# Kernel tuning notes

Hardware: AMD Instinct MI355X
Metric: run time of the kernel (lower is better)

## Reference

```python
import jax, jax.numpy as jnp
import numpy as np

N_NODES = 50000
N_EDGES = 1600000
IN_C, HID_C, OUT_C = 64, 64, 7


def setup_inputs() -> dict:
    key = jax.random.key(0)
    ks = jax.random.split(key, 8)
    x = jax.random.normal(ks[0], (N_NODES, IN_C), dtype=jnp.float32)
    edge_index = jax.random.randint(ks[1], (2, N_EDGES), 0, N_NODES, dtype=jnp.int64)
    s_in = 1.0 / np.sqrt(IN_C)
    s_hid = 1.0 / np.sqrt(HID_C)
    W1 = jax.random.normal(ks[2], (HID_C, IN_C), dtype=jnp.float32) * s_in
    b1 = jnp.zeros((HID_C,), dtype=jnp.float32)
    W2 = jax.random.normal(ks[3], (HID_C, HID_C), dtype=jnp.float32) * s_hid
    b2 = jnp.zeros((HID_C,), dtype=jnp.float32)
    W3 = jax.random.normal(ks[4], (OUT_C, HID_C), dtype=jnp.float32) * s_hid
    b3 = jnp.zeros((OUT_C,), dtype=jnp.float32)
    return {"x": x, "edge_index": edge_index, "W1": W1, "b1": b1,
            "W2": W2, "b2": b2, "W3": W3, "b3": b3}


def _gcn_conv(x, src, dst, W, b):
    # GCNConv(normalize=False): lin -> sum-aggregate over incoming edges -> +bias
    h = x @ W.T                                   # [N, out]
    msg = h[src]                                  # gather source features [E, out]
    agg = jax.ops.segment_sum(msg, dst, num_segments=N_NODES)  # scatter-add
    return agg + b


def reference(x, edge_index, W1, b1, W2, b2, W3, b3):
    src, dst = edge_index[0], edge_index[1]
    h = jax.nn.relu(_gcn_conv(x, src, dst, W1, b1))   # dropout is identity in eval
    h = jax.nn.relu(_gcn_conv(h, src, dst, W2, b2))
    h = _gcn_conv(h, src, dst, W3, b3)
    return jax.nn.log_softmax(h, axis=-1)
```

## Files before the change

kernel.cpp:

```cpp
#include <hip/hip_runtime.h>
#include <math.h>

#define N_NODES 50000
#define N_EDGES 1600000
#define C 64
#define OUTC 7

#define NB 196
#define BCAP 10240
#define CHUNK 8192

#define ZROW N_NODES

typedef __attribute__((ext_vector_type(8))) short bf16x8;
typedef __attribute__((ext_vector_type(4))) float f32x4;
typedef __attribute__((ext_vector_type(2))) float f32x2;

__device__ __forceinline__ unsigned int pk_bf16(float a, float b) {
    unsigned int ua = __float_as_uint(a);
    ua = (ua + 0x7FFFu + ((ua >> 16) & 1u)) >> 16;
    unsigned int ub = __float_as_uint(b);
    ub = (ub + 0x7FFFu + ((ub >> 16) & 1u)) >> 16;
    return ua | (ub << 16);
}

union U4B8 { uint4 u; bf16x8 s; };

__global__ __launch_bounds__(256) void prep(const float* __restrict__ W1,
                                            const float* __restrict__ W2,
                                            unsigned int* __restrict__ Wb1,
                                            unsigned int* __restrict__ Wb2,
                                            int* __restrict__ gcursor) {
    const int b = blockIdx.x;
    const int tid = threadIdx.x;
    if (b < 8) {
        int idx = b * 256 + tid;
        float2 v = ((const float2*)W1)[idx];
        Wb1[idx] = pk_bf16(v.x, v.y);
    } else if (b < 16) {
        int idx = (b - 8) * 256 + tid;
        float2 v = ((const float2*)W2)[idx];
        Wb2[idx] = pk_bf16(v.x, v.y);
    } else {
        if (tid < NB) gcursor[tid] = 0;
    }
}

__global__ __launch_bounds__(256) void bin_kernel(const int* __restrict__ src,
                                                  const int* __restrict__ dst,
                                                  unsigned int* __restrict__ buckets,
                                                  int* __restrict__ gcursor) {
    __shared__ unsigned int staged[CHUNK];
    __shared__ int hist[NB], scanb[NB], cur[NB], baseb[NB];
    const int tid = threadIdx.x;
    const int base = blockIdx.x * CHUNK;
    int n = N_EDGES - base; if (n > CHUNK) n = CHUNK;

    for (int b = tid; b < NB; b += 256) { hist[b] = 0; cur[b] = 0; }
    __syncthreads();

    const int4* src4 = (const int4*)(src + base);
    const int4* dst4 = (const int4*)(dst + base);
    unsigned int v[32];
    int nv = n >> 2;
#pragma unroll
    for (int k = 0; k < 8; ++k) {
        int i4 = k * 256 + tid;
        if (i4 < nv) {
            int4 s4 = src4[i4];
            int4 d4 = dst4[i4];
            unsigned int d0 = (unsigned int)d4.x, d1 = (unsigned int)d4.y;
            unsigned int d2 = (unsigned int)d4.z, d3 = (unsigned int)d4.w;
            v[k * 4 + 0] = (d0 << 16) | (unsigned int)s4.x;
            v[k * 4 + 1] = (d1 << 16) | (unsigned int)s4.y;
            v[k * 4 + 2] = (d2 << 16) | (unsigned int)s4.z;
            v[k * 4 + 3] = (d3 << 16) | (unsigned int)s4.w;
            atomicAdd(&hist[d0 >> 8], 1);
            atomicAdd(&hist[d1 >> 8], 1);
            atomicAdd(&hist[d2 >> 8], 1);
            atomicAdd(&hist[d3 >> 8], 1);
        }
    }
    __syncthreads();
    if (tid == 0) {
        int run = 0;
        for (int b = 0; b < NB; ++b) { scanb[b] = run; run += hist[b]; }
    }
    __syncthreads();
#pragma unroll
    for (int k = 0; k < 8; ++k) {
        int i4 = k * 256 + tid;
        if (i4 < nv) {
#pragma unroll
            for (int q = 0; q < 4; ++q) {
                unsigned int w = v[k * 4 + q];
                int b = w >> 24;
                int p = scanb[b] + atomicAdd(&cur[b], 1);
                staged[p] = w;
            }
        }
    }
    __syncthreads();
    if (tid < NB) baseb[tid] = atomicAdd(&gcursor[tid], hist[tid]);
    __syncthreads();
    for (int i = tid; i < n; i += 256) {
        unsigned int w = staged[i];
        int b = w >> 24;
        buckets[(size_t)b * BCAP + baseb[b] + (i - scanb[b])] = w;
    }
}

__global__ __launch_bounds__(256) void build_csr(const unsigned int* __restrict__ buckets,
                                                 const int* __restrict__ gcursor,
                                                 unsigned int* __restrict__ csr,
                                                 int* __restrict__ off) {
    __shared__ int hist[256], part[256], offx[256], cur[256];
    __shared__ int gl[NB];
    __shared__ int s_cnt, s_base;
    const int tid = threadIdx.x;
    const int b = blockIdx.x;

    hist[tid] = 0;
    cur[tid] = 0;
    if (tid < NB) gl[tid] = gcursor[tid];
    __syncthreads();
    if (tid == 0) {
        int bs = 0;
        for (int i = 0; i < b; ++i) bs += gl[i];
        s_base = bs;
        s_cnt = gl[b];
    }
    __syncthreads();
    const int cnt = s_cnt;
    const int gbase = s_base;
    const unsigned int* bk = buckets + (size_t)b * BCAP;

    for (int i = tid; i < cnt; i += 256) {
        atomicAdd(&hist[(bk[i] >> 16) & 255], 1);
    }
    __syncthreads();
    part[tid] = hist[tid];
    __syncthreads();
    for (int d = 1; d < 256; d <<= 1) {
        int t = (tid >= d) ? part[tid - d] : 0;
        __syncthreads();
        part[tid] += t;
        __syncthreads();
    }
    offx[tid] = (tid == 0) ? 0 : part[tid - 1];
    __syncthreads();
    int node = b * 256 + tid;
    if (node < N_NODES) off[node] = gbase + offx[tid];
    if (b == NB - 1 && tid == 0) off[N_NODES] = gbase + cnt;
    for (int i = tid; i < cnt; i += 256) {
        unsigned int w = bk[i];
        int dl = (w >> 16) & 255;
        int p = offx[dl] + atomicAdd(&cur[dl], 1);
        csr[gbase + p] = w & 0xFFFFu;
    }
}


__global__ __launch_bounds__(256) void linear64_mfma_x(const float* __restrict__ x,
                                                       const unsigned int* __restrict__ Wb,
                                                       unsigned int* __restrict__ out) {
    if (blockIdx.x == 0 && threadIdx.x < 32)
        out[(size_t)ZROW * 32 + threadIdx.x] = 0u;
    const int wave = threadIdx.x >> 6;
    const int lane = threadIdx.x & 63;
    const int quad = lane >> 4;
    const int l16  = lane & 15;
    const int rbase = blockIdx.x * 64 + wave * 16;
    if (rbase >= N_NODES) return;

    U4B8 bfrag[4][2];
#pragma unroll
    for (int ct = 0; ct < 4; ++ct)
#pragma unroll
        for (int kt = 0; kt < 2; ++kt)
            bfrag[ct][kt].u = *(const uint4*)(Wb + (ct * 16 + l16) * 32 + kt * 16 + quad * 4);

    U4B8 afrag[2];
#pragma unroll
    for (int kt = 0; kt < 2; ++kt) {
        const float4* xp = (const float4*)(x + (size_t)(rbase + l16) * 64 + kt * 32 + quad * 8);
        float4 f0 = xp[0];
        float4 f1 = xp[1];
        afrag[kt].u.x = pk_bf16(f0.x, f0.y);
        afrag[kt].u.y = pk_bf16(f0.z, f0.w);
        afrag[kt].u.z = pk_bf16(f1.x, f1.y);
        afrag[kt].u.w = pk_bf16(f1.z, f1.w);
    }

    f32x4 acc[4];
#pragma unroll
    for (int ct = 0; ct < 4; ++ct) {
        f32x4 z = {0.f, 0.f, 0.f, 0.f};
        z = __builtin_amdgcn_mfma_f32_16x16x32_bf16(afrag[0].s, bfrag[ct][0].s, z, 0, 0, 0);
        z = __builtin_amdgcn_mfma_f32_16x16x32_bf16(afrag[1].s, bfrag[ct][1].s, z, 0, 0, 0);
        acc[ct] = z;
    }

    const int colp = l16 >> 1;
    const bool even = (l16 & 1) == 0;
#pragma unroll
    for (int ct = 0; ct < 4; ++ct) {
#pragma unroll
        for (int i = 0; i < 4; ++i) {
            float v = acc[ct][i];
            float p = __shfl_xor(v, 1, 64);
            if (even) {
                int row = rbase + quad * 4 + i;
                out[(size_t)row * 32 + ct * 8 + colp] = pk_bf16(v, p);
            }
        }
    }
}

__global__ __launch_bounds__(256) void linear64_mfma(const unsigned int* __restrict__ in,
                                                     const unsigned int* __restrict__ Wb,
                                                     unsigned int* __restrict__ out) {
    if (blockIdx.x == 0 && threadIdx.x < 32)
        out[(size_t)ZROW * 32 + threadIdx.x] = 0u;
    const int wave = threadIdx.x >> 6;
    const int lane = threadIdx.x & 63;
    const int quad = lane >> 4;
    const int l16  = lane & 15;
    const int rbase = blockIdx.x * 64 + wave * 16;
    if (rbase >= N_NODES) return;

    U4B8 bfrag[4][2];
#pragma unroll
    for (int ct = 0; ct < 4; ++ct)
#pragma unroll
        for (int kt = 0; kt < 2; ++kt)
            bfrag[ct][kt].u = *(const uint4*)(Wb + (ct * 16 + l16) * 32 + kt * 16 + quad * 4);

    U4B8 afrag[2];
#pragma unroll
    for (int kt = 0; kt < 2; ++kt)
        afrag[kt].u = *(const uint4*)(in + (size_t)(rbase + l16) * 32 + kt * 16 + quad * 4);

    f32x4 acc[4];
#pragma unroll
    for (int ct = 0; ct < 4; ++ct) {
        f32x4 z = {0.f, 0.f, 0.f, 0.f};
        z = __builtin_amdgcn_mfma_f32_16x16x32_bf16(afrag[0].s, bfrag[ct][0].s, z, 0, 0, 0);
        z = __builtin_amdgcn_mfma_f32_16x16x32_bf16(afrag[1].s, bfrag[ct][1].s, z, 0, 0, 0);
        acc[ct] = z;
    }

    const int colp = l16 >> 1;
    const bool even = (l16 & 1) == 0;
#pragma unroll
    for (int ct = 0; ct < 4; ++ct) {
#pragma unroll
        for (int i = 0; i < 4; ++i) {
            float v = acc[ct][i];
            float p = __shfl_xor(v, 1, 64);
            if (even) {
                int row = rbase + quad * 4 + i;
                out[(size_t)row * 32 + ct * 8 + colp] = pk_bf16(v, p);
            }
        }
    }
}

#define ACC8(v)                                                              \
    do {                                                                     \
        s01 += (f32x2){__uint_as_float((v).x << 16),                         \
                       __uint_as_float((v).x & 0xFFFF0000u)};                \
        s23 += (f32x2){__uint_as_float((v).y << 16),                         \
                       __uint_as_float((v).y & 0xFFFF0000u)};                \
        s45 += (f32x2){__uint_as_float((v).z << 16),                         \
                       __uint_as_float((v).z & 0xFFFF0000u)};                \
        s67 += (f32x2){__uint_as_float((v).w << 16),                         \
                       __uint_as_float((v).w & 0xFFFF0000u)};                \
    } while (0)

__global__ __launch_bounds__(256) void gather64b(const int* __restrict__ off,
                                                 const unsigned int* __restrict__ csr_src,
                                                 const unsigned int* __restrict__ tb,
                                                 const float* __restrict__ b,
                                                 unsigned int* __restrict__ hb) {
    int node = blockIdx.x * 4 + (threadIdx.x >> 6);
    if (node >= N_NODES) return;
    const int lane = threadIdx.x & 63;
    const int slot = lane >> 3;
    const int ch8  = lane & 7;
    int e0 = off[node], e1 = off[node + 1];
    const uint4* t4 = (const uint4*)tb;
    f32x2 s01 = {0.f, 0.f}, s23 = {0.f, 0.f}, s45 = {0.f, 0.f}, s67 = {0.f, 0.f};
    for (int e = e0; e < e1; e += 64) {
        unsigned int a[8];
#pragma unroll
        for (int k = 0; k < 8; ++k) {
            int i = e + slot + k * 8;
            unsigned int av = csr_src[i];
            a[k] = (i < e1) ? av : ZROW;
        }
        uint4 v[8];
#pragma unroll
        for (int k = 0; k < 8; ++k) v[k] = t4[(size_t)a[k] * 8 + ch8];
#pragma unroll
        for (int k = 0; k < 8; ++k) ACC8(v[k]);
    }
    float s[8] = {s01.x, s01.y, s23.x, s23.y, s45.x, s45.y, s67.x, s67.y};
#pragma unroll
    for (int d = 8; d <= 32; d <<= 1) {
#pragma unroll
        for (int j = 0; j < 8; ++j) s[j] += __shfl_xor(s[j], d, 64);
    }
    if (lane < 8) {
        const float4 b0 = ((const float4*)b)[ch8 * 2];
        const float4 b1 = ((const float4*)b)[ch8 * 2 + 1];
        float r0 = fmaxf(s[0] + b0.x, 0.f);
        float r1 = fmaxf(s[1] + b0.y, 0.f);
        float r2 = fmaxf(s[2] + b0.z, 0.f);
        float r3 = fmaxf(s[3] + b0.w, 0.f);
        float r4 = fmaxf(s[4] + b1.x, 0.f);
        float r5 = fmaxf(s[5] + b1.y, 0.f);
        float r6 = fmaxf(s[6] + b1.z, 0.f);
        float r7 = fmaxf(s[7] + b1.w, 0.f);
        uint4 w;
        w.x = pk_bf16(r0, r1);
        w.y = pk_bf16(r2, r3);
        w.z = pk_bf16(r4, r5);
        w.w = pk_bf16(r6, r7);
        ((uint4*)(hb + (size_t)node * 32))[ch8] = w;
    }
}

__global__ __launch_bounds__(256) void gather64b_w3(const int* __restrict__ off,
                                                    const unsigned int* __restrict__ csr_src,
                                                    const unsigned int* __restrict__ tb,
                                                    const float* __restrict__ b,
                                                    const float* __restrict__ W3,
                                                    unsigned int* __restrict__ t3) {
    if (blockIdx.x == 0 && threadIdx.x < 4)
        t3[(size_t)ZROW * 4 + threadIdx.x] = 0u;
    int node = blockIdx.x * 4 + (threadIdx.x >> 6);
    if (node >= N_NODES) return;
    const int lane = threadIdx.x & 63;
    const int slot = lane >> 3;
    const int ch8  = lane & 7;
    int e0 = off[node], e1 = off[node + 1];
    const uint4* t4 = (const uint4*)tb;
    f32x2 s01 = {0.f, 0.f}, s23 = {0.f, 0.f}, s45 = {0.f, 0.f}, s67 = {0.f, 0.f};
    for (int e = e0; e < e1; e += 64) {
        unsigned int a[8];
#pragma unroll
        for (int k = 0; k < 8; ++k) {
            int i = e + slot + k * 8;
            unsigned int av = csr_src[i];
            a[k] = (i < e1) ? av : ZROW;
        }
        uint4 v[8];
#pragma unroll
        for (int k = 0; k < 8; ++k) v[k] = t4[(size_t)a[k] * 8 + ch8];
#pragma unroll
        for (int k = 0; k < 8; ++k) ACC8(v[k]);
    }
    float s[8] = {s01.x, s01.y, s23.x, s23.y, s45.x, s45.y, s67.x, s67.y};
#pragma unroll
    for (int d = 8; d <= 32; d <<= 1) {
#pragma unroll
        for (int j = 0; j < 8; ++j) s[j] += __shfl_xor(s[j], d, 64);
    }
    const float4 b0 = ((const float4*)b)[ch8 * 2];
    const float4 b1 = ((const float4*)b)[ch8 * 2 + 1];
    float r[8];
    r[0] = fmaxf(s[0] + b0.x, 0.f);
    r[1] = fmaxf(s[1] + b0.y, 0.f);
    r[2] = fmaxf(s[2] + b0.z, 0.f);
    r[3] = fmaxf(s[3] + b0.w, 0.f);
    r[4] = fmaxf(s[4] + b1.x, 0.f);
    r[5] = fmaxf(s[5] + b1.y, 0.f);
    r[6] = fmaxf(s[6] + b1.z, 0.f);
    r[7] = fmaxf(s[7] + b1.w, 0.f);
    float p[7];
#pragma unroll
    for (int j = 0; j < 7; ++j) {
        const float4 wa = *(const float4*)(W3 + j * 64 + ch8 * 8);
        const float4 wb = *(const float4*)(W3 + j * 64 + ch8 * 8 + 4);
        float t = r[0] * wa.x + r[1] * wa.y + r[2] * wa.z + r[3] * wa.w
                + r[4] * wb.x + r[5] * wb.y + r[6] * wb.z + r[7] * wb.w;
        t += __shfl_xor(t, 1, 64);
        t += __shfl_xor(t, 2, 64);
        t += __shfl_xor(t, 4, 64);
        p[j] = t;
    }
    if (lane == 0) {
        uint4 w;
        w.x = pk_bf16(p[0], p[1]);
        w.y = pk_bf16(p[2], p[3]);
        w.z = pk_bf16(p[4], p[5]);
        w.w = pk_bf16(p[6], 0.f);
        *(uint4*)(t3 + (size_t)node * 4) = w;
    }
}

__global__ __launch_bounds__(256) void gather7_lsm(const int* __restrict__ off,
                                                   const unsigned int* __restrict__ csr_src,
                                                   const unsigned int* __restrict__ t3,
                                                   const float* __restrict__ b,
                                                   float* __restrict__ out) {
    int node = blockIdx.x * 4 + (threadIdx.x >> 6);
    if (node >= N_NODES) return;
    const int lane = threadIdx.x & 63;
    const int slot = lane >> 1;
    const int h    = lane & 1;
    int e0 = off[node], e1 = off[node + 1];
    const uint2* t2 = (const uint2*)t3;
    float sx = 0.f, sy = 0.f, sz = 0.f, sw = 0.f;
    for (int e = e0; e < e1; e += 64) {
        int i0 = e + slot;
        int i1 = e + 32 + slot;
        unsigned int a0 = csr_src[i0];
        unsigned int a1 = csr_src[i1];
        a0 = (i0 < e1) ? a0 : ZROW;
        a1 = (i1 < e1) ? a1 : ZROW;
        uint2 v0 = t2[(size_t)a0 * 2 + h];
        uint2 v1 = t2[(size_t)a1 * 2 + h];
        sx += __uint_as_float(v0.x << 16);
        sy += __uint_as_float(v0.x & 0xFFFF0000u);
        sz += __uint_as_float(v0.y << 16);
        sw += __uint_as_float(v0.y & 0xFFFF0000u);
        sx += __uint_as_float(v1.x << 16);
        sy += __uint_as_float(v1.x & 0xFFFF0000u);
        sz += __uint_as_float(v1.y << 16);
        sw += __uint_as_float(v1.y & 0xFFFF0000u);
    }
#pragma unroll
    for (int d = 2; d <= 32; d <<= 1) {
        sx += __shfl_xor(sx, d, 64); sy += __shfl_xor(sy, d, 64);
        sz += __shfl_xor(sz, d, 64); sw += __shfl_xor(sw, d, 64);
    }
    float z0 = sx + b[h * 4 + 0];
    float z1 = sy + b[h * 4 + 1];
    float z2 = sz + b[h * 4 + 2];
    float z3 = (h == 0) ? (sw + b[3]) : -1e30f;
    float m = fmaxf(fmaxf(z0, z1), fmaxf(z2, z3));
    m = fmaxf(m, __shfl_xor(m, 1, 64));
    float ex = __expf(z0 - m) + __expf(z1 - m) + __expf(z2 - m) + __expf(z3 - m);
    ex += __shfl_xor(ex, 1, 64);
    float l = m + __logf(ex);
    if (lane < 2) {
        float* o = out + (size_t)node * 7 + h * 4;
        o[0] = z0 - l; o[1] = z1 - l; o[2] = z2 - l;
        if (h == 0) o[3] = z3 - l;
    }
}

extern "C" void kernel_launch(void* const* d_in, const int* in_sizes, int n_in,
                              void* d_out, int out_size, void* d_ws, size_t ws_size,
                              hipStream_t stream) {
    const float* x  = (const float*)d_in[0];
    const int*   ei = (const int*)d_in[1];
    const float* W1 = (const float*)d_in[2];
    const float* b1 = (const float*)d_in[3];
    const float* W2 = (const float*)d_in[4];
    const float* b2 = (const float*)d_in[5];
    const float* W3 = (const float*)d_in[6];
    const float* b3 = (const float*)d_in[7];
    float* out = (float*)d_out;

    const int* src = ei;
    const int* dst = ei + N_EDGES;

    float* A = (float*)d_ws;
    float* B = A + (size_t)N_NODES * C;
    unsigned int* csr = (unsigned int*)(B + (size_t)N_NODES * C);
    int* off     = (int*)(csr + N_EDGES);
    int* gcursor = off + N_NODES + 8;
    unsigned int* Wb1 = (unsigned int*)(gcursor + 256);
    unsigned int* Wb2 = Wb1 + 2048;
    unsigned int* buckets = (unsigned int*)A;
    unsigned int* Abf     = (unsigned int*)A;
    unsigned int* Hbf     = (unsigned int*)B;
    unsigned int* T3      = (unsigned int*)B;

    const int mfmagrid = (N_NODES + 63) / 64;
    const int ngrid    = (N_NODES + 3) / 4;

    prep<<<17, 256, 0, stream>>>(W1, W2, Wb1, Wb2, gcursor);

    bin_kernel<<<(N_EDGES + CHUNK - 1) / CHUNK, 256, 0, stream>>>(src, dst, buckets, gcursor);
    build_csr<<<NB, 256, 0, stream>>>(buckets, gcursor, csr, off);

    linear64_mfma_x<<<mfmagrid, 256, 0, stream>>>(x, Wb1, Abf);
    gather64b<<<ngrid, 256, 0, stream>>>(off, csr, Abf, b1, Hbf);

    linear64_mfma<<<mfmagrid, 256, 0, stream>>>(Hbf, Wb2, Abf);

    gather64b_w3<<<ngrid, 256, 0, stream>>>(off, csr, Abf, b2, W3, T3);

    gather7_lsm<<<ngrid, 256, 0, stream>>>(off, csr, T3, b3, out);
}
```

Baseline: 226.1 us.

## Process four nodes per wave in gather kernels with batched first-chunk loads

Result: no change. 229.5 us (+1.5%).

```diff
diff --git a/kernel.cpp b/kernel.cpp
--- a/kernel.cpp
+++ b/kernel.cpp
@@ -283,51 +283,78 @@
                                                  const unsigned int* __restrict__ tb,
                                                  const float* __restrict__ b,
                                                  unsigned int* __restrict__ hb) {
-    int node = blockIdx.x * 4 + (threadIdx.x >> 6);
-    if (node >= N_NODES) return;
+    const int wave = threadIdx.x >> 6;
     const int lane = threadIdx.x & 63;
     const int slot = lane >> 3;
     const int ch8  = lane & 7;
-    int e0 = off[node], e1 = off[node + 1];
+    const int n0 = (blockIdx.x * 4 + wave) * 4;
+    if (n0 >= N_NODES) return;
     const uint4* t4 = (const uint4*)tb;
-    f32x2 s01 = {0.f, 0.f}, s23 = {0.f, 0.f}, s45 = {0.f, 0.f}, s67 = {0.f, 0.f};
-    for (int e = e0; e < e1; e += 64) {
-        unsigned int a[8];
-#pragma unroll
-        for (int k = 0; k < 8; ++k) {
-            int i = e + slot + k * 8;
+
+    int eb[5];
+#pragma unroll
+    for (int k = 0; k < 5; ++k) eb[k] = off[n0 + k];
+
+    unsigned int idx[4][4];
+#pragma unroll
+    for (int k = 0; k < 4; ++k) {
+        int e0 = eb[k], e1 = eb[k + 1];
+#pragma unroll
+        for (int j = 0; j < 4; ++j) {
+            int i = e0 + slot + j * 8;
             unsigned int av = csr_src[i];
-            a[k] = (i < e1) ? av : ZROW;
-        }
-        uint4 v[8];
-#pragma unroll
-        for (int k = 0; k < 8; ++k) v[k] = t4[(size_t)a[k] * 8 + ch8];
-#pragma unroll
-        for (int k = 0; k < 8; ++k) ACC8(v[k]);
-    }
-    float s[8] = {s01.x, s01.y, s23.x, s23.y, s45.x, s45.y, s67.x, s67.y};
-#pragma unroll
-    for (int d = 8; d <= 32; d <<= 1) {
-#pragma unroll
-        for (int j = 0; j < 8; ++j) s[j] += __shfl_xor(s[j], d, 64);
-    }
-    if (lane < 8) {
-        const float4 b0 = ((const float4*)b)[ch8 * 2];
-        const float4 b1 = ((const float4*)b)[ch8 * 2 + 1];
-        float r0 = fmaxf(s[0] + b0.x, 0.f);
-        float r1 = fmaxf(s[1] + b0.y, 0.f);
-        float r2 = fmaxf(s[2] + b0.z, 0.f);
-        float r3 = fmaxf(s[3] + b0.w, 0.f);
-        float r4 = fmaxf(s[4] + b1.x, 0.f);
-        float r5 = fmaxf(s[5] + b1.y, 0.f);
-        float r6 = fmaxf(s[6] + b1.z, 0.f);
-        float r7 = fmaxf(s[7] + b1.w, 0.f);
-        uint4 w;
-        w.x = pk_bf16(r0, r1);
-        w.y = pk_bf16(r2, r3);
-        w.z = pk_bf16(r4, r5);
-        w.w = pk_bf16(r6, r7);
-        ((uint4*)(hb + (size_t)node * 32))[ch8] = w;
+            idx[k][j] = (i < e1) ? av : ZROW;
+        }
+    }
+    uint4 tv[4][4];
+#pragma unroll
+    for (int k = 0; k < 4; ++k)
+#pragma unroll
+        for (int j = 0; j < 4; ++j)
+            tv[k][j] = t4[(size_t)idx[k][j] * 8 + ch8];
+
+#pragma unroll
+    for (int k = 0; k < 4; ++k) {
+        f32x2 s01 = {0.f, 0.f}, s23 = {0.f, 0.f}, s45 = {0.f, 0.f}, s67 = {0.f, 0.f};
+        ACC8(tv[k][0]);
+        ACC8(tv[k][1]);
+        ACC8(tv[k][2]);
+        ACC8(tv[k][3]);
+        const int e1 = eb[k + 1];
+        for (int e = eb[k] + 32; e < e1; e += 32) {
+#pragma unroll
+            for (int j = 0; j < 4; ++j) {
+                int i = e + slot + j * 8;
+                unsigned int av = csr_src[i];
+                av = (i < e1) ? av : ZROW;
+                uint4 v = t4[(size_t)av * 8 + ch8];
+                ACC8(v);
+            }
+        }
+        float s[8] = {s01.x, s01.y, s23.x, s23.y, s45.x, s45.y, s67.x, s67.y};
+#pragma unroll
+        for (int d = 8; d <= 32; d <<= 1) {
+#pragma unroll
+            for (int j = 0; j < 8; ++j) s[j] += __shfl_xor(s[j], d, 64);
+        }
+        if (lane < 8) {
+            const float4 b0 = ((const float4*)b)[ch8 * 2];
+            const float4 b1 = ((const float4*)b)[ch8 * 2 + 1];
+            float r0 = fmaxf(s[0] + b0.x, 0.f);
+            float r1 = fmaxf(s[1] + b0.y, 0.f);
+            float r2 = fmaxf(s[2] + b0.z, 0.f);
+            float r3 = fmaxf(s[3] + b0.w, 0.f);
+            float r4 = fmaxf(s[4] + b1.x, 0.f);
+            float r5 = fmaxf(s[5] + b1.y, 0.f);
+            float r6 = fmaxf(s[6] + b1.z, 0.f);
+            float r7 = fmaxf(s[7] + b1.w, 0.f);
+            uint4 w;
+            w.x = pk_bf16(r0, r1);
+            w.y = pk_bf16(r2, r3);
+            w.z = pk_bf16(r4, r5);
+            w.w = pk_bf16(r6, r7);
+            ((uint4*)(hb + (size_t)(n0 + k) * 32))[ch8] = w;
+        }
     }
 }
 
@@ -339,64 +366,91 @@
                                                     unsigned int* __restrict__ t3) {
     if (blockIdx.x == 0 && threadIdx.x < 4)
         t3[(size_t)ZROW * 4 + threadIdx.x] = 0u;
-    int node = blockIdx.x * 4 + (threadIdx.x >> 6);
-    if (node >= N_NODES) return;
+    const int wave = threadIdx.x >> 6;
     const int lane = threadIdx.x & 63;
     const int slot = lane >> 3;
     const int ch8  = lane & 7;
-    int e0 = off[node], e1 = off[node + 1];
+    const int n0 = (blockIdx.x * 4 + wave) * 4;
+    if (n0 >= N_NODES) return;
     const uint4* t4 = (const uint4*)tb;
-    f32x2 s01 = {0.f, 0.f}, s23 = {0.f, 0.f}, s45 = {0.f, 0.f}, s67 = {0.f, 0.f};
-    for (int e = e0; e < e1; e += 64) {
-        unsigned int a[8];
-#pragma unroll
-        for (int k = 0; k < 8; ++k) {
-            int i = e + slot + k * 8;
+
+    int eb[5];
+#pragma unroll
+    for (int k = 0; k < 5; ++k) eb[k] = off[n0 + k];
+
+    unsigned int idx[4][4];
+#pragma unroll
+    for (int k = 0; k < 4; ++k) {
+        int e0 = eb[k], e1 = eb[k + 1];
+#pragma unroll
+        for (int j = 0; j < 4; ++j) {
+            int i = e0 + slot + j * 8;
             unsigned int av = csr_src[i];
-            a[k] = (i < e1) ? av : ZROW;
-        }
-        uint4 v[8];
-#pragma unroll
-        for (int k = 0; k < 8; ++k) v[k] = t4[(size_t)a[k] * 8 + ch8];
-#pragma unroll
-        for (int k = 0; k < 8; ++k) ACC8(v[k]);
-    }
-    float s[8] = {s01.x, s01.y, s23.x, s23.y, s45.x, s45.y, s67.x, s67.y};
-#pragma unroll
-    for (int d = 8; d <= 32; d <<= 1) {
-#pragma unroll
-        for (int j = 0; j < 8; ++j) s[j] += __shfl_xor(s[j], d, 64);
-    }
-    const float4 b0 = ((const float4*)b)[ch8 * 2];
-    const float4 b1 = ((const float4*)b)[ch8 * 2 + 1];
-    float r[8];
-    r[0] = fmaxf(s[0] + b0.x, 0.f);
-    r[1] = fmaxf(s[1] + b0.y, 0.f);
-    r[2] = fmaxf(s[2] + b0.z, 0.f);
-    r[3] = fmaxf(s[3] + b0.w, 0.f);
-    r[4] = fmaxf(s[4] + b1.x, 0.f);
-    r[5] = fmaxf(s[5] + b1.y, 0.f);
-    r[6] = fmaxf(s[6] + b1.z, 0.f);
-    r[7] = fmaxf(s[7] + b1.w, 0.f);
-    float p[7];
-#pragma unroll
-    for (int j = 0; j < 7; ++j) {
-        const float4 wa = *(const float4*)(W3 + j * 64 + ch8 * 8);
-        const float4 wb = *(const float4*)(W3 + j * 64 + ch8 * 8 + 4);
-        float t = r[0] * wa.x + r[1] * wa.y + r[2] * wa.z + r[3] * wa.w
-                + r[4] * wb.x + r[5] * wb.y + r[6] * wb.z + r[7] * wb.w;
-        t += __shfl_xor(t, 1, 64);
-        t += __shfl_xor(t, 2, 64);
-        t += __shfl_xor(t, 4, 64);
-        p[j] = t;
-    }
-    if (lane == 0) {
-        uint4 w;
-        w.x = pk_bf16(p[0], p[1]);
-        w.y = pk_bf16(p[2], p[3]);
-        w.z = pk_bf16(p[4], p[5]);
-        w.w = pk_bf16(p[6], 0.f);
-        *(uint4*)(t3 + (size_t)node * 4) = w;
+            idx[k][j] = (i < e1) ? av : ZROW;
+        }
+    }
+    uint4 tv[4][4];
+#pragma unroll
+    for (int k = 0; k < 4; ++k)
+#pragma unroll
+        for (int j = 0; j < 4; ++j)
+            tv[k][j] = t4[(size_t)idx[k][j] * 8 + ch8];
+
+#pragma unroll
+    for (int k = 0; k < 4; ++k) {
+        f32x2 s01 = {0.f, 0.f}, s23 = {0.f, 0.f}, s45 = {0.f, 0.f}, s67 = {0.f, 0.f};
+        ACC8(tv[k][0]);
+        ACC8(tv[k][1]);
+        ACC8(tv[k][2]);
+        ACC8(tv[k][3]);
+        const int e1 = eb[k + 1];
+        for (int e = eb[k] + 32; e < e1; e += 32) {
+#pragma unroll
+            for (int j = 0; j < 4; ++j) {
+                int i = e + slot + j * 8;
+                unsigned int av = csr_src[i];
+                av = (i < e1) ? av : ZROW;
+                uint4 v = t4[(size_t)av * 8 + ch8];
+                ACC8(v);
+            }
+        }
+        float s[8] = {s01.x, s01.y, s23.x, s23.y, s45.x, s45.y, s67.x, s67.y};
+#pragma unroll
+        for (int d = 8; d <= 32; d <<= 1) {
+#pragma unroll
+            for (int j = 0; j < 8; ++j) s[j] += __shfl_xor(s[j], d, 64);
+        }
+        const float4 b0 = ((const float4*)b)[ch8 * 2];
+        const float4 b1 = ((const float4*)b)[ch8 * 2 + 1];
+        float r[8];
+        r[0] = fmaxf(s[0] + b0.x, 0.f);
+        r[1] = fmaxf(s[1] + b0.y, 0.f);
+        r[2] = fmaxf(s[2] + b0.z, 0.f);
+        r[3] = fmaxf(s[3] + b0.w, 0.f);
+        r[4] = fmaxf(s[4] + b1.x, 0.f);
+        r[5] = fmaxf(s[5] + b1.y, 0.f);
+        r[6] = fmaxf(s[6] + b1.z, 0.f);
+        r[7] = fmaxf(s[7] + b1.w, 0.f);
+        float p[7];
+#pragma unroll
+        for (int j = 0; j < 7; ++j) {
+            const float4 wa = *(const float4*)(W3 + j * 64 + ch8 * 8);
+            const float4 wb = *(const float4*)(W3 + j * 64 + ch8 * 8 + 4);
+            float t = r[0] * wa.x + r[1] * wa.y + r[2] * wa.z + r[3] * wa.w
+                    + r[4] * wb.x + r[5] * wb.y + r[6] * wb.z + r[7] * wb.w;
+            t += __shfl_xor(t, 1, 64);
+            t += __shfl_xor(t, 2, 64);
+            t += __shfl_xor(t, 4, 64);
+            p[j] = t;
+        }
+        if (lane == 0) {
+            uint4 w;
+            w.x = pk_bf16(p[0], p[1]);
+            w.y = pk_bf16(p[2], p[3]);
+            w.z = pk_bf16(p[4], p[5]);
+            w.w = pk_bf16(p[6], 0.f);
+            *(uint4*)(t3 + (size_t)(n0 + k) * 4) = w;
+        }
     }
 }
 
@@ -405,50 +459,65 @@
                                                    const unsigned int* __restrict__ t3,
                                                    const float* __restrict__ b,
                                                    float* __restrict__ out) {
-    int node = blockIdx.x * 4 + (threadIdx.x >> 6);
-    if (node >= N_NODES) return;
+    const int wave = threadIdx.x >> 6;
     const int lane = threadIdx.x & 63;
     const int slot = lane >> 1;
     const int h    = lane & 1;
-    int e0 = off[node], e1 = off[node + 1];
+    const int n0 = (blockIdx.x * 4 + wave) * 4;
+    if (n0 >= N_NODES) return;
     const uint2* t2 = (const uint2*)t3;
-    float sx = 0.f, sy = 0.f, sz = 0.f, sw = 0.f;
-    for (int e = e0; e < e1; e += 64) {
-        int i0 = e + slot;
-        int i1 = e + 32 + slot;
-        unsigned int a0 = csr_src[i0];
-        unsigned int a1 = csr_src[i1];
-        a0 = (i0 < e1) ? a0 : ZROW;
-        a1 = (i1 < e1) ? a1 : ZROW;
-        uint2 v0 = t2[(size_t)a0 * 2 + h];
-        uint2 v1 = t2[(size_t)a1 * 2 + h];
-        sx += __uint_as_float(v0.x << 16);
-        sy += __uint_as_float(v0.x & 0xFFFF0000u);
-        sz += __uint_as_float(v0.y << 16);
-        sw += __uint_as_float(v0.y & 0xFFFF0000u);
-        sx += __uint_as_float(v1.x << 16);
-        sy += __uint_as_float(v1.x & 0xFFFF0000u);
-        sz += __uint_as_float(v1.y << 16);
-        sw += __uint_as_float(v1.y & 0xFFFF0000u);
-    }
-#pragma unroll
-    for (int d = 2; d <= 32; d <<= 1) {
-        sx += __shfl_xor(sx, d, 64); sy += __shfl_xor(sy, d, 64);
-        sz += __shfl_xor(sz, d, 64); sw += __shfl_xor(sw, d, 64);
-    }
-    float z0 = sx + b[h * 4 + 0];
-    float z1 = sy + b[h * 4 + 1];
-    float z2 = sz + b[h * 4 + 2];
-    float z3 = (h == 0) ? (sw + b[3]) : -1e30f;
-    float m = fmaxf(fmaxf(z0, z1), fmaxf(z2, z3));
-    m = fmaxf(m, __shfl_xor(m, 1, 64));
-    float ex = __expf(z0 - m) + __expf(z1 - m) + __expf(z2 - m) + __expf(z3 - m);
-    ex += __shfl_xor(ex, 1, 64);
-    float l = m + __logf(ex);
-    if (lane < 2) {
-        float* o = out + (size_t)node * 7 + h * 4;
-        o[0] = z0 - l; o[1] = z1 - l; o[2] = z2 - l;
-        if (h == 0) o[3] = z3 - l;
+
+    int eb[5];
+#pragma unroll
+    for (int k = 0; k < 5; ++k) eb[k] = off[n0 + k];
+
+    unsigned int idx[4];
+#pragma unroll
+    for (int k = 0; k < 4; ++k) {
+        int i = eb[k] + slot;
+        unsigned int av = csr_src[i];
+        idx[k] = (i < eb[k + 1]) ? av : ZROW;
+    }
+    uint2 tv[4];
+#pragma unroll
+    for (int k = 0; k < 4; ++k) tv[k] = t2[(size_t)idx[k] * 2 + h];
+
+#pragma unroll
+    for (int k = 0; k < 4; ++k) {
+        float sx = __uint_as_float(tv[k].x << 16);
+        float sy = __uint_as_float(tv[k].x & 0xFFFF0000u);
+        float sz = __uint_as_float(tv[k].y << 16);
+        float sw = __uint_as_float(tv[k].y & 0xFFFF0000u);
+        const int e1 = eb[k + 1];
+        for (int e = eb[k] + 32; e < e1; e += 32) {
+            int i = e + slot;
+            unsigned int av = csr_src[i];
+            av = (i < e1) ? av : ZROW;
+            uint2 v = t2[(size_t)av * 2 + h];
+            sx += __uint_as_float(v.x << 16);
+            sy += __uint_as_float(v.x & 0xFFFF0000u);
+            sz += __uint_as_float(v.y << 16);
+            sw += __uint_as_float(v.y & 0xFFFF0000u);
+        }
+#pragma unroll
+        for (int d = 2; d <= 32; d <<= 1) {
+            sx += __shfl_xor(sx, d, 64); sy += __shfl_xor(sy, d, 64);
+            sz += __shfl_xor(sz, d, 64); sw += __shfl_xor(sw, d, 64);
+        }
+        float z0 = sx + b[h * 4 + 0];
+        float z1 = sy + b[h * 4 + 1];
+        float z2 = sz + b[h * 4 + 2];
+        float z3 = (h == 0) ? (sw + b[3]) : -1e30f;
+        float m = fmaxf(fmaxf(z0, z1), fmaxf(z2, z3));
+        m = fmaxf(m, __shfl_xor(m, 1, 64));
+        float ex = __expf(z0 - m) + __expf(z1 - m) + __expf(z2 - m) + __expf(z3 - m);
+        ex += __shfl_xor(ex, 1, 64);
+        float l = m + __logf(ex);
+        if (lane < 2) {
+            float* o = out + (size_t)(n0 + k) * 7 + h * 4;
+            o[0] = z0 - l; o[1] = z1 - l; o[2] = z2 - l;
+            if (h == 0) o[3] = z3 - l;
+        }
     }
 }
 
@@ -481,7 +550,7 @@
     unsigned int* T3      = (unsigned int*)B;
 
     const int mfmagrid = (N_NODES + 63) / 64;
-    const int ngrid    = (N_NODES + 3) / 4;
+    const int ngrid4   = (N_NODES + 15) / 16;
 
     prep<<<17, 256, 0, stream>>>(W1, W2, Wb1, Wb2, gcursor);
 
@@ -489,11 +558,11 @@
     build_csr<<<NB, 256, 0, stream>>>(buckets, gcursor, csr, off);
 
     linear64_mfma_x<<<mfmagrid, 256, 0, stream>>>(x, Wb1, Abf);
-    gather64b<<<ngrid, 256, 0, stream>>>(off, csr, Abf, b1, Hbf);
+    gather64b<<<ngrid4, 256, 0, stream>>>(off, csr, Abf, b1, Hbf);
 
     linear64_mfma<<<mfmagrid, 256, 0, stream>>>(Hbf, Wb2, Abf);
 
-    gather64b_w3<<<ngrid, 256, 0, stream>>>(off, csr, Abf, b2, W3, T3);
-
-    gather7_lsm<<<ngrid, 256, 0, stream>>>(off, csr, T3, b3, out);
-}
+    gather64b_w3<<<ngrid4, 256, 0, stream>>>(off, csr, Abf, b2, W3, T3);
+
+    gather7_lsm<<<ngrid4, 256, 0, stream>>>(off, csr, T3, b3, out);
+}
```
